# Optimization experiments

Measured on AMD Instinct MI355X. Metric: run time of the kernel, lower is better.

Reference implementation:

```python
import jax, jax.numpy as jnp
import numpy as np

N, H = 8192, 1024

def setup_inputs() -> dict:
    key = jax.random.key(0)
    ks = jax.random.split(key, 7)
    s = 1.0 / np.sqrt(H)
    return {
        "input_tensor": jax.random.normal(ks[0], (N, H), dtype=jnp.float32),
        "Wq": jax.random.uniform(ks[1], (H, H), dtype=jnp.float32, minval=-s, maxval=s),
        "bq": jax.random.uniform(ks[2], (H,), dtype=jnp.float32, minval=-s, maxval=s),
        "Wk": jax.random.uniform(ks[3], (H, H), dtype=jnp.float32, minval=-s, maxval=s),
        "bk": jax.random.uniform(ks[4], (H,), dtype=jnp.float32, minval=-s, maxval=s),
        "Wv": jax.random.uniform(ks[5], (H, H), dtype=jnp.float32, minval=-s, maxval=s),
        "bv": jax.random.uniform(ks[6], (H,), dtype=jnp.float32, minval=-s, maxval=s),
    }

def reference(input_tensor, Wq, bq, Wk, bk, Wv, bv):
    # torch nn.Linear: x @ W.T + b
    q = input_tensor @ Wq.T + bq  # [N, H]
    k = input_tensor @ Wk.T + bk  # [N, H]
    v = input_tensor @ Wv.T + bv  # [N, H]
    scale = jnp.sqrt(jnp.asarray(input_tensor.shape[1], dtype=q.dtype))
    # (q @ k.T / sqrt(H)) @ v  -- no softmax; same math as original
    scores = (q @ k.T) / scale  # [N, N]
    return scores @ v  # [N, H]
```

## Files before the change

### kernel.cpp

```cpp
#include <hip/hip_runtime.h>
#include <hip/hip_bf16.h>
#include <stdint.h>
#include <stddef.h>

typedef __bf16 bf16_t;
typedef __bf16 bf16x4 __attribute__((ext_vector_type(4)));
typedef __bf16 bf16x8 __attribute__((ext_vector_type(8)));
typedef float  floatx4 __attribute__((ext_vector_type(4)));

#define TK 32

__global__ void prep_x(const float* __restrict__ x, bf16_t* __restrict__ xb,
                       bf16_t* __restrict__ xbT, float* __restrict__ s,
                       int SEQ, int H) {
    __shared__ bf16_t tile[64][72];
    __shared__ float csum[64];
    const int t = threadIdx.x;
    const int n0 = blockIdx.x * 64, k0 = blockIdx.y * 64;
    const int c4 = t & 15;
    const int rbase = t >> 4;
    float a0 = 0.f, a1 = 0.f, a2 = 0.f, a3 = 0.f;
    if (t < 64) csum[t] = 0.f;
    #pragma unroll
    for (int p = 0; p < 4; ++p) {
        const int r = rbase + 16 * p;
        const size_t gidx = (size_t)(n0 + r) * H + k0 + c4 * 4;
        float4 f = *(const float4*)(x + gidx);
        bf16x4 o;
        o.x = (bf16_t)f.x; o.y = (bf16_t)f.y;
        o.z = (bf16_t)f.z; o.w = (bf16_t)f.w;
        *(bf16x4*)(xb + gidx) = o;
        *(bf16x4*)&tile[r][c4 * 4] = o;
        a0 += f.x; a1 += f.y; a2 += f.z; a3 += f.w;
    }
    __syncthreads();
    atomicAdd(&csum[c4 * 4 + 0], a0);
    atomicAdd(&csum[c4 * 4 + 1], a1);
    atomicAdd(&csum[c4 * 4 + 2], a2);
    atomicAdd(&csum[c4 * 4 + 3], a3);
    #pragma unroll
    for (int p = 0; p < 2; ++p) {
        const int q = t + 256 * p;
        const int kk = q >> 3;
        const int n8 = (q & 7) * 8;
        bf16x8 v;
        #pragma unroll
        for (int u = 0; u < 8; ++u) v[u] = tile[n8 + u][kk];
        *(bf16x8*)(xbT + (size_t)(k0 + kk) * SEQ + n0 + n8) = v;
    }
    __syncthreads();
    if (t < 64) atomicAdd(s + k0 + t, csum[t]);
}

__global__ void prep_w(const float* __restrict__ Wk, bf16_t* __restrict__ Wkb,
                       const float* __restrict__ Wv, bf16_t* __restrict__ Wvb,
                       const float* __restrict__ Wq, bf16_t* __restrict__ WqTb,
                       float* __restrict__ svec) {
    __shared__ bf16_t tile[64][72];
    const int b = blockIdx.x;
    const int t = threadIdx.x;
    if (b == 2304) {
        *(float4*)(svec + t * 4) = float4{0.f, 0.f, 0.f, 0.f};
        return;
    }
    if (b < 2048) {
        const float* s = (b < 1024) ? Wk : Wv;
        bf16_t* d = (b < 1024) ? Wkb : Wvb;
        const int base = (b & 1023) * 1024 + t * 4;
        float4 f = *(const float4*)(s + base);
        bf16x4 o;
        o.x = (bf16_t)f.x; o.y = (bf16_t)f.y;
        o.z = (bf16_t)f.z; o.w = (bf16_t)f.w;
        *(bf16x4*)(d + base) = o;
    } else {
        const int bb = b - 2048;
        const int r0 = (bb & 15) * 64, c0 = (bb >> 4) * 64;
        const int c4 = t & 15;
        const int rbase = t >> 4;
        #pragma unroll
        for (int p = 0; p < 4; ++p) {
            const int r = rbase + 16 * p;
            float4 f = *(const float4*)(Wq + (size_t)(r0 + r) * 1024 + c0 + c4 * 4);
            bf16x4 o;
            o.x = (bf16_t)f.x; o.y = (bf16_t)f.y;
            o.z = (bf16_t)f.z; o.w = (bf16_t)f.w;
            *(bf16x4*)&tile[r][c4 * 4] = o;
        }
        __syncthreads();
        #pragma unroll
        for (int p = 0; p < 2; ++p) {
            const int q = t + 256 * p;
            const int cc = q >> 3;
            const int r8 = (q & 7) * 8;
            bf16x8 v;
            #pragma unroll
            for (int u = 0; u < 8; ++u) v[u] = tile[r8 + u][cc];
            *(bf16x8*)(WqTb + (size_t)(c0 + cc) * 1024 + r0 + r8) = v;
        }
    }
}

__global__ void matvec2(const bf16_t* __restrict__ M0,
                        const bf16_t* __restrict__ M1,
                        const float* __restrict__ v,
                        float* __restrict__ y0, float* __restrict__ y1,
                        int ncols) {
    const int lane = threadIdx.x & 63;
    const int row = blockIdx.x * 4 + (threadIdx.x >> 6);
    const bf16_t* mp;
    float* y;
    if (row < 1024) { mp = M0 + (size_t)row * ncols;          y = y0 + row; }
    else            { mp = M1 + (size_t)(row - 1024) * ncols; y = y1 + row - 1024; }
    float acc = 0.f;
    for (int a = lane * 8; a < ncols; a += 512) {
        bf16x8 m8 = *(const bf16x8*)(mp + a);
        #pragma unroll
        for (int u = 0; u < 8; ++u) acc += (float)m8[u] * v[a + u];
    }
    #pragma unroll
    for (int off = 32; off; off >>= 1) acc += __shfl_down(acc, off);
    if (lane == 0) *y = acc;
}

__global__ void matvec_bf16(const bf16_t* __restrict__ M,
                            const float* __restrict__ v,
                            float* __restrict__ y, int ncols, float scale) {
    const int lane = threadIdx.x & 63;
    const int row = blockIdx.x * 4 + (threadIdx.x >> 6);
    const bf16_t* mp = M + (size_t)row * ncols;
    float acc = 0.f;
    for (int a = lane * 8; a < ncols; a += 512) {
        bf16x8 m8 = *(const bf16x8*)(mp + a);
        #pragma unroll
        for (int u = 0; u < 8; ++u) acc += (float)m8[u] * v[a + u];
    }
    #pragma unroll
    for (int off = 32; off; off >>= 1) acc += __shfl_down(acc, off);
    if (lane == 0) y[row] = acc * scale;
}

__global__ void reduce_splitk(const float* __restrict__ part,
                              bf16_t* __restrict__ dst, int n, int nsplit,
                              float scale) {
    int i = (blockIdx.x * blockDim.x + threadIdx.x) * 4;
    if (i < n) {
        float4 ssum = *(const float4*)(part + i);
        for (int z = 1; z < nsplit; ++z) {
            float4 p = *(const float4*)(part + (size_t)z * n + i);
            ssum.x += p.x; ssum.y += p.y; ssum.z += p.z; ssum.w += p.w;
        }
        bf16x4 o;
        o.x = (bf16_t)(ssum.x * scale); o.y = (bf16_t)(ssum.y * scale);
        o.z = (bf16_t)(ssum.z * scale); o.w = (bf16_t)(ssum.w * scale);
        *(bf16x4*)(dst + i) = o;
    }
}

template <int TMp, int TNp, int MODE, typename OutT>
__global__ __launch_bounds__(256, 2) void gemm_bt(
    const bf16_t* __restrict__ A,
    const bf16_t* __restrict__ B,
    OutT* __restrict__ C,
    const float* __restrict__ p1, const float* __restrict__ p2,
    const float* __restrict__ p3, const float* __restrict__ p4,
    int M, int N, int K, int kChunk, float scale, float cN)
{
    __shared__ __align__(16) bf16_t As[TMp * TK];
    __shared__ __align__(16) bf16_t Bs[TNp * TK];
    constexpr int MF = TMp / 32;
    constexpr int NF = TNp / 32;
    constexpr int nA = TMp / 64;
    constexpr int nB = TNp / 64;

    const int tid  = threadIdx.x;
    const int lane = tid & 63;
    const int wave = tid >> 6;
    const int wm   = wave >> 1;
    const int wn   = wave & 1;

    const int bm = blockIdx.y * TMp;
    const int bn = blockIdx.x * TNp;
    const int k0 = blockIdx.z * kChunk;
    C += (size_t)blockIdx.z * M * N;

    floatx4 acc[MF][NF] = {};

    const int fr = lane & 15;
    const int fk = (lane >> 4) * 8;

    for (int kt = k0; kt < k0 + kChunk; kt += TK) {
        #pragma unroll
        for (int p = 0; p < nA; ++p) {
            const int c = tid + 256 * p;
            const int r = c >> 2, o = (c & 3) * 8;
            __builtin_amdgcn_global_load_lds(
                (const __attribute__((address_space(1))) void*)
                    (A + (size_t)(bm + r) * K + kt + o),
                (__attribute__((address_space(3))) void*)&As[c * 8], 16, 0, 0);
        }
        #pragma unroll
        for (int p = 0; p < nB; ++p) {
            const int c = tid + 256 * p;
            const int r = c >> 2, o = (c & 3) * 8;
            __builtin_amdgcn_global_load_lds(
                (const __attribute__((address_space(1))) void*)
                    (B + (size_t)(bn + r) * K + kt + o),
                (__attribute__((address_space(3))) void*)&Bs[c * 8], 16, 0, 0);
        }
        __syncthreads();

        bf16x8 af[MF], bg[NF];
        #pragma unroll
        for (int i = 0; i < MF; ++i)
            af[i] = *(const bf16x8*)&As[(wm * (TMp / 2) + i * 16 + fr) * TK + fk];
        #pragma unroll
        for (int j = 0; j < NF; ++j)
            bg[j] = *(const bf16x8*)&Bs[(wn * (TNp / 2) + j * 16 + fr) * TK + fk];
        #pragma unroll
        for (int i = 0; i < MF; ++i) {
            #pragma unroll
            for (int j = 0; j < NF; ++j) {
                acc[i][j] = __builtin_amdgcn_mfma_f32_16x16x32_bf16(
                    af[i], bg[j], acc[i][j], 0, 0, 0);
            }
        }
        __syncthreads();
    }

    const int rq = (lane >> 4) * 4;
    #pragma unroll
    for (int i = 0; i < MF; ++i) {
        #pragma unroll
        for (int j = 0; j < NF; ++j) {
            const int col = bn + wn * (TNp / 2) + j * 16 + fr;
            #pragma unroll
            for (int r = 0; r < 4; ++r) {
                const int row = bm + wm * (TMp / 2) + i * 16 + rq + r;
                float v = acc[i][j][r] * scale;
                if (MODE == 1) v += p1[col];
                if (MODE == 2) v += p1[row] * p2[col] + p3[row] * p4[col]
                                  + cN * p1[row] * p4[col];
                C[(size_t)row * N + col] = (OutT)v;
            }
        }
    }
}

extern "C" void kernel_launch(void* const* d_in, const int* in_sizes, int n_in,
                              void* d_out, int out_size, void* d_ws, size_t ws_size,
                              hipStream_t stream) {
    const int SEQ = 8192;
    const int H   = 1024;

    const float* x  = (const float*)d_in[0];
    const float* Wq = (const float*)d_in[1];
    const float* bq = (const float*)d_in[2];
    const float* Wk = (const float*)d_in[3];
    const float* bk = (const float*)d_in[4];
    const float* Wv = (const float*)d_in[5];
    const float* bv = (const float*)d_in[6];
    float* out = (float*)d_out;

    const size_t MI = 1024 * 1024;
    char* ws = (char*)d_ws;
    bf16_t* xb   = (bf16_t*)(ws);
    bf16_t* xbT  = (bf16_t*)(ws + 16 * MI);
    bf16_t* Wkb  = (bf16_t*)(ws + 32 * MI);
    bf16_t* Wvb  = (bf16_t*)(ws + 34 * MI);
    bf16_t* WqTb = (bf16_t*)(ws + 36 * MI);
    bf16_t* Gb   = (bf16_t*)(ws + 38 * MI);
    bf16_t* S1b  = (bf16_t*)(ws + 40 * MI);
    bf16_t* Ttb  = (bf16_t*)(ws + 42 * MI);
    bf16_t* Utb  = (bf16_t*)(ws + 44 * MI);
    float*  svec = (float*)(ws + 46 * MI);
    float*  kv1  = svec + 1024;
    float*  wvs  = svec + 2048;
    float*  cvec = svec + 3072;
    float*  part = (float*)(ws + 48 * MI);

    dim3 blk(256);
    const float inv32 = 1.0f / 32.0f;
    const int nHH = H * H;
    const float* nil = nullptr;

    prep_w<<<dim3(2305), blk, 0, stream>>>(Wk, Wkb, Wv, Wvb, Wq, WqTb, svec);
    prep_x<<<dim3(SEQ / 64, H / 64), blk, 0, stream>>>(x, xb, xbT, svec, SEQ, H);
    matvec2<<<dim3(512), blk, 0, stream>>>(Wkb, Wvb, svec, kv1, wvs, H);
    gemm_bt<128, 128, 0, float><<<dim3(8, 8, 16), blk, 0, stream>>>(
        xbT, xbT, part, nil, nil, nil, nil, H, H, SEQ, SEQ / 16, 1.0f, 0.f);
    reduce_splitk<<<dim3(nHH / 1024), blk, 0, stream>>>(part, Gb, nHH, 16, 1.0f);
    gemm_bt<64, 64, 0, bf16_t><<<dim3(16, 16), blk, 0, stream>>>(
        Wvb, Gb, S1b, nil, nil, nil, nil, H, H, H, H, 1.0f, 0.f);
    gemm_bt<64, 64, 2, bf16_t><<<dim3(16, 16), blk, 0, stream>>>(
        S1b, Wkb, Ttb, bv, kv1, wvs, bk, H, H, H, H, 1.0f, (float)SEQ);
    matvec_bf16<<<dim3(H / 4), blk, 0, stream>>>(Ttb, bq, cvec, H, inv32);
    gemm_bt<64, 64, 0, bf16_t><<<dim3(16, 16), blk, 0, stream>>>(
        Ttb, WqTb, Utb, nil, nil, nil, nil, H, H, H, H, inv32, 0.f);
    gemm_bt<128, 128, 1, float><<<dim3(8, 64), blk, 0, stream>>>(
        xb, Utb, out, cvec, nil, nil, nil, SEQ, H, H, H, 1.0f, 0.f);
}
```

Before: 232.4 us.

## Split-K the small HxH GEMMs with bf16 partials and swizzled block mapping

The three 1024x1024 GEMMs move from 64x64 tiles with 256 blocks to 128x128 tiles split 8 ways along K, giving 512 blocks. Partials are written in bf16 and summed by new vectorized reduce kernels, one of which applies the rank-1 bias correction that used to live in the GEMM epilogue. The large Gram GEMM also switches to bf16 partials with a 1D swizzled launch that interleaves split indices, and the final GEMM uses a swizzled block order. Storing partials in bf16 halves reduction traffic but adds rounding error, and the extra reduce launches add overhead.

```diff
diff --git a/kernel.cpp b/kernel.cpp
--- a/kernel.cpp
+++ b/kernel.cpp
@@ -139,31 +139,58 @@
     if (lane == 0) y[row] = acc * scale;
 }
 
-__global__ void reduce_splitk(const float* __restrict__ part,
-                              bf16_t* __restrict__ dst, int n, int nsplit,
-                              float scale) {
-    int i = (blockIdx.x * blockDim.x + threadIdx.x) * 4;
+__global__ void reduce_bf16(const bf16_t* __restrict__ part,
+                            bf16_t* __restrict__ dst, int n, int nsplit,
+                            float scale) {
+    int i = (blockIdx.x * blockDim.x + threadIdx.x) * 8;
     if (i < n) {
-        float4 ssum = *(const float4*)(part + i);
-        for (int z = 1; z < nsplit; ++z) {
-            float4 p = *(const float4*)(part + (size_t)z * n + i);
-            ssum.x += p.x; ssum.y += p.y; ssum.z += p.z; ssum.w += p.w;
-        }
-        bf16x4 o;
-        o.x = (bf16_t)(ssum.x * scale); o.y = (bf16_t)(ssum.y * scale);
-        o.z = (bf16_t)(ssum.z * scale); o.w = (bf16_t)(ssum.w * scale);
-        *(bf16x4*)(dst + i) = o;
-    }
-}
-
-template <int TMp, int TNp, int MODE, typename OutT>
+        float acc[8] = {};
+        for (int z = 0; z < nsplit; ++z) {
+            bf16x8 p = *(const bf16x8*)(part + (size_t)z * n + i);
+            #pragma unroll
+            for (int u = 0; u < 8; ++u) acc[u] += (float)p[u];
+        }
+        bf16x8 o;
+        #pragma unroll
+        for (int u = 0; u < 8; ++u) o[u] = (bf16_t)(acc[u] * scale);
+        *(bf16x8*)(dst + i) = o;
+    }
+}
+
+__global__ void reduce_bf16_rank1(const bf16_t* __restrict__ part,
+                                  bf16_t* __restrict__ dst, int n, int nsplit,
+                                  const float* __restrict__ bv,
+                                  const float* __restrict__ kv1,
+                                  const float* __restrict__ wvs,
+                                  const float* __restrict__ bk,
+                                  float cN, int Hdim) {
+    int i = (blockIdx.x * blockDim.x + threadIdx.x) * 8;
+    if (i < n) {
+        float acc[8] = {};
+        for (int z = 0; z < nsplit; ++z) {
+            bf16x8 p = *(const bf16x8*)(part + (size_t)z * n + i);
+            #pragma unroll
+            for (int u = 0; u < 8; ++u) acc[u] += (float)p[u];
+        }
+        const int j = i / Hdim, ii = i % Hdim;
+        const float bvj = bv[j], wvsj = wvs[j];
+        bf16x8 o;
+        #pragma unroll
+        for (int u = 0; u < 8; ++u) {
+            float v = acc[u] + bvj * kv1[ii + u] + (wvsj + cN * bvj) * bk[ii + u];
+            o[u] = (bf16_t)v;
+        }
+        *(bf16x8*)(dst + i) = o;
+    }
+}
+
+template <int TMp, int TNp, int MODE, int SWZ, typename OutT>
 __global__ __launch_bounds__(256, 2) void gemm_bt(
     const bf16_t* __restrict__ A,
     const bf16_t* __restrict__ B,
     OutT* __restrict__ C,
-    const float* __restrict__ p1, const float* __restrict__ p2,
-    const float* __restrict__ p3, const float* __restrict__ p4,
-    int M, int N, int K, int kChunk, float scale, float cN)
+    const float* __restrict__ p1,
+    int M, int N, int K, int kChunk, float scale)
 {
     __shared__ __align__(16) bf16_t As[TMp * TK];
     __shared__ __align__(16) bf16_t Bs[TNp * TK];
@@ -178,10 +205,27 @@
     const int wm   = wave >> 1;
     const int wn   = wave & 1;
 
-    const int bm = blockIdx.y * TMp;
-    const int bn = blockIdx.x * TNp;
-    const int k0 = blockIdx.z * kChunk;
-    C += (size_t)blockIdx.z * M * N;
+    int bm, bn, z;
+    if (SWZ == 0) {
+        bm = blockIdx.y * TMp; bn = blockIdx.x * TNp; z = blockIdx.z;
+    } else if (SWZ == 1) {
+        const int L = blockIdx.x;
+        z = ((L & 7) << 1) | (L >> 9);
+        const int mn = (L >> 3) & 63;
+        bm = (mn >> 3) * TMp; bn = (mn & 7) * TNp;
+    } else if (SWZ == 2) {
+        const int L = blockIdx.x;
+        bm = ((L & 7) * 8 + ((L >> 3) & 7)) * TMp;
+        bn = (L >> 6) * TNp;
+        z = 0;
+    } else {
+        const int L = blockIdx.x;
+        z = L & 7;
+        const int mn = L >> 3;
+        bm = (mn >> 3) * TMp; bn = (mn & 7) * TNp;
+    }
+    const int k0 = z * kChunk;
+    C += (size_t)z * M * N;
 
     floatx4 acc[MF][NF] = {};
 
@@ -238,8 +282,6 @@
                 const int row = bm + wm * (TMp / 2) + i * 16 + rq + r;
                 float v = acc[i][j][r] * scale;
                 if (MODE == 1) v += p1[col];
-                if (MODE == 2) v += p1[row] * p2[col] + p3[row] * p4[col]
-                                  + cN * p1[row] * p4[col];
                 C[(size_t)row * N + col] = (OutT)v;
             }
         }
@@ -276,26 +318,31 @@
     float*  kv1  = svec + 1024;
     float*  wvs  = svec + 2048;
     float*  cvec = svec + 3072;
-    float*  part = (float*)(ws + 48 * MI);
+    bf16_t* part = (bf16_t*)(ws + 48 * MI);
 
     dim3 blk(256);
     const float inv32 = 1.0f / 32.0f;
     const int nHH = H * H;
+    const int rgrid = nHH / 8 / 256;
     const float* nil = nullptr;
 
     prep_w<<<dim3(2305), blk, 0, stream>>>(Wk, Wkb, Wv, Wvb, Wq, WqTb, svec);
     prep_x<<<dim3(SEQ / 64, H / 64), blk, 0, stream>>>(x, xb, xbT, svec, SEQ, H);
     matvec2<<<dim3(512), blk, 0, stream>>>(Wkb, Wvb, svec, kv1, wvs, H);
-    gemm_bt<128, 128, 0, float><<<dim3(8, 8, 16), blk, 0, stream>>>(
-        xbT, xbT, part, nil, nil, nil, nil, H, H, SEQ, SEQ / 16, 1.0f, 0.f);
-    reduce_splitk<<<dim3(nHH / 1024), blk, 0, stream>>>(part, Gb, nHH, 16, 1.0f);
-    gemm_bt<64, 64, 0, bf16_t><<<dim3(16, 16), blk, 0, stream>>>(
-        Wvb, Gb, S1b, nil, nil, nil, nil, H, H, H, H, 1.0f, 0.f);
-    gemm_bt<64, 64, 2, bf16_t><<<dim3(16, 16), blk, 0, stream>>>(
-        S1b, Wkb, Ttb, bv, kv1, wvs, bk, H, H, H, H, 1.0f, (float)SEQ);
+    gemm_bt<128, 128, 0, 1, bf16_t><<<dim3(1024), blk, 0, stream>>>(
+        xbT, xbT, part, nil, H, H, SEQ, SEQ / 16, 1.0f);
+    reduce_bf16<<<dim3(rgrid), blk, 0, stream>>>(part, Gb, nHH, 16, 1.0f);
+    gemm_bt<128, 128, 0, 3, bf16_t><<<dim3(512), blk, 0, stream>>>(
+        Wvb, Gb, part, nil, H, H, H, H / 8, 1.0f);
+    reduce_bf16<<<dim3(rgrid), blk, 0, stream>>>(part, S1b, nHH, 8, 1.0f);
+    gemm_bt<128, 128, 0, 3, bf16_t><<<dim3(512), blk, 0, stream>>>(
+        S1b, Wkb, part, nil, H, H, H, H / 8, 1.0f);
+    reduce_bf16_rank1<<<dim3(rgrid), blk, 0, stream>>>(
+        part, Ttb, nHH, 8, bv, kv1, wvs, bk, (float)SEQ, H);
     matvec_bf16<<<dim3(H / 4), blk, 0, stream>>>(Ttb, bq, cvec, H, inv32);
-    gemm_bt<64, 64, 0, bf16_t><<<dim3(16, 16), blk, 0, stream>>>(
-        Ttb, WqTb, Utb, nil, nil, nil, nil, H, H, H, H, inv32, 0.f);
-    gemm_bt<128, 128, 1, float><<<dim3(8, 64), blk, 0, stream>>>(
-        xb, Utb, out, cvec, nil, nil, nil, SEQ, H, H, H, 1.0f, 0.f);
-}
+    gemm_bt<128, 128, 0, 3, bf16_t><<<dim3(512), blk, 0, stream>>>(
+        Ttb, WqTb, part, nil, H, H, H, H / 8, 1.0f);
+    reduce_bf16<<<dim3(rgrid), blk, 0, stream>>>(part, Utb, nHH, 8, inv32);
+    gemm_bt<128, 128, 1, 2, float><<<dim3(512), blk, 0, stream>>>(
+        xb, Utb, out, cvec, SEQ, H, H, H, 1.0f);
+}
```

After: 230.9 us. No clear change (-0.6%).
